# Performance work log

Hardware: AMD Instinct MI355X
Metric: run time of the kernel (lower is better)

Reference implementation:

```python
import jax, jax.numpy as jnp
import numpy as np


def _gat_layer(x, W, att_l, att_r, b, src, dst, num_nodes, heads, out_feat, concat):
    # x: [N, in], W: [in, H*F]
    xl = (x @ W).reshape(num_nodes, heads, out_feat)          # [N, H, F]
    a_l = jnp.sum(xl * att_l, axis=2)                          # [N, H]
    a_r = jnp.sum(xl * att_r, axis=2)                          # [N, H]
    # edge scores: alpha_j (source, att_l) + alpha_i (target, att_r)
    e = a_l[src] + a_r[dst]                                    # [E, H]
    e = jax.nn.leaky_relu(e, 0.2)
    # segment softmax over destination-node neighborhoods
    e_max = jax.ops.segment_max(e, dst, num_segments=num_nodes)
    e_exp = jnp.exp(e - e_max[dst])
    denom = jax.ops.segment_sum(e_exp, dst, num_segments=num_nodes)
    alpha = e_exp / (denom[dst] + 1e-16)                       # [E, H]
    # weighted gather + scatter-add aggregation
    msg = alpha[:, :, None] * xl[src]                          # [E, H, F]
    out = jax.ops.segment_sum(msg, dst, num_segments=num_nodes)  # [N, H, F]
    if concat:
        out = out.reshape(num_nodes, heads * out_feat)
    else:
        out = out.mean(axis=1)                                 # [N, F]
    return out + b


def setup_inputs() -> dict:
    key = jax.random.key(0)
    ks = jax.random.split(key, 8)
    N, E = 50000, 800000
    in_dim, hidden, out_dim, H = 128, 8, 64, 8
    x = jax.random.normal(ks[0], (N, in_dim), dtype=jnp.float32)
    edge_index = jax.random.randint(ks[1], (2, E), 0, N, dtype=jnp.int64)
    s = 0.1
    return {
        "x": x,
        "edge_index": edge_index,
        "W1": jax.random.normal(ks[2], (in_dim, hidden * H), dtype=jnp.float32) * s,
        "att_l1": jax.random.normal(ks[3], (1, H, hidden), dtype=jnp.float32) * s,
        "att_r1": jax.random.normal(ks[4], (1, H, hidden), dtype=jnp.float32) * s,
        "b1": jnp.zeros((hidden * H,), dtype=jnp.float32),
        "W2": jax.random.normal(ks[5], (hidden * H, out_dim * H), dtype=jnp.float32) * s,
        "att_l2": jax.random.normal(ks[6], (1, H, out_dim), dtype=jnp.float32) * s,
        "att_r2": jax.random.normal(ks[7], (1, H, out_dim), dtype=jnp.float32) * s,
        "b2": jnp.zeros((1, out_dim), dtype=jnp.float32),
    }


def reference(x, edge_index, W1, att_l1, att_r1, b1, W2, att_l2, att_r2, b2):
    N = x.shape[0]
    H = att_l1.shape[1]
    src, dst = edge_index[0], edge_index[1]
    h = _gat_layer(x, W1, att_l1, att_r1, b1, src, dst, N, H, att_l1.shape[2], concat=True)
    h = jax.nn.relu(h)
    out = _gat_layer(h, W2, att_l2, att_r2, b2, src, dst, N, H, att_l2.shape[2], concat=False)
    return out
```

## Files before the change

kernel.cpp:

```cpp
#include <hip/hip_runtime.h>
#include <stdint.h>

#define NT 256
#define CHUNK 4096
#define BSHIFT 8

typedef __attribute__((ext_vector_type(8))) short bf16x8;
typedef __attribute__((ext_vector_type(4))) float f32x4;

__device__ __forceinline__ float lrelu(float x) { return x > 0.f ? x : 0.2f * x; }

__device__ __forceinline__ float b2f(unsigned short u) {
  union { unsigned int i; float f; } v; v.i = ((unsigned int)u) << 16; return v.f;
}
__device__ __forceinline__ unsigned short f2b(float f) {
  unsigned int u = __float_as_uint(f);
  return (unsigned short)((u + 0x7fffu + ((u >> 16) & 1u)) >> 16);
}

__global__ void detect_kernel(const int* __restrict__ ei, int* __restrict__ flag, int twoE) {
  __shared__ int any;
  if (threadIdx.x == 0) any = 0;
  __syncthreads();
  int n = twoE < 4096 ? twoE : 4096;
  for (int i = threadIdx.x * 2 + 1; i < n; i += 2 * NT)
    if (ei[i] != 0) any = 1;
  __syncthreads();
  if (threadIdx.x == 0) *flag = any;
}

__global__ void cvt_edges_kernel(const void* __restrict__ ei, int* __restrict__ out,
                                 const int* __restrict__ flag, int twoE) {
  int i = blockIdx.x * NT + threadIdx.x;
  if (i >= twoE) return;
  if (*flag) out[i] = ((const int*)ei)[i];
  else       out[i] = (int)((const long long*)ei)[i];
}

__global__ void zero2_kernel(int* __restrict__ a, int* __restrict__ b, int n) {
  int i = blockIdx.x * NT + threadIdx.x;
  if (i < n) { a[i] = 0; b[i] = 0; }
}

__global__ void scan1_kernel(const int* __restrict__ in, int* __restrict__ bsum, int n) {
  __shared__ int sm[NT];
  int idx = blockIdx.x * NT + threadIdx.x;
  sm[threadIdx.x] = (idx < n) ? in[idx] : 0;
  __syncthreads();
  for (int s = NT / 2; s > 0; s >>= 1) {
    if (threadIdx.x < s) sm[threadIdx.x] += sm[threadIdx.x + s];
    __syncthreads();
  }
  if (threadIdx.x == 0) bsum[blockIdx.x] = sm[0];
}

__global__ void scan2_kernel(const int* __restrict__ bsum, int* __restrict__ boff, int SB) {
  __shared__ int sm[NT];
  int t = threadIdx.x;
  int v = (t < SB) ? bsum[t] : 0;
  sm[t] = v;
  __syncthreads();
  for (int s = 1; s < NT; s <<= 1) {
    int add = (t >= s) ? sm[t - s] : 0;
    __syncthreads();
    sm[t] += add;
    __syncthreads();
  }
  if (t < SB) boff[t] = sm[t] - v;
}

__global__ void scan3_kernel(const int* __restrict__ in, const int* __restrict__ boff,
                             int* __restrict__ out, int n) {
  __shared__ int sm[NT];
  int idx = blockIdx.x * NT + threadIdx.x;
  int v = (idx < n) ? in[idx] : 0;
  sm[threadIdx.x] = v;
  __syncthreads();
  for (int s = 1; s < NT; s <<= 1) {
    int add = (threadIdx.x >= s) ? sm[threadIdx.x - s] : 0;
    __syncthreads();
    sm[threadIdx.x] += add;
    __syncthreads();
  }
  if (idx <= n) out[idx] = boff[blockIdx.x] + sm[threadIdx.x] - v;
}

__global__ void bincount_kernel(const int* __restrict__ dst, int* __restrict__ blkcnt,
                                int E, int nblk, int nbk) {
  __shared__ int cnt[256];
  int b = blockIdx.x;
  for (int i = threadIdx.x; i < nbk; i += NT) cnt[i] = 0;
  __syncthreads();
  int beg = b * CHUNK;
  int end = beg + CHUNK < E ? beg + CHUNK : E;
  for (int i = beg + threadIdx.x; i < end; i += NT)
    atomicAdd(&cnt[dst[i] >> BSHIFT], 1);
  __syncthreads();
  for (int i = threadIdx.x; i < nbk; i += NT) blkcnt[i * nblk + b] = cnt[i];
}

__global__ void binwrite_kernel(const int* __restrict__ src, const int* __restrict__ dst,
                                const int* __restrict__ base, long long* __restrict__ binned,
                                int E, int nblk, int nbk) {
  __shared__ int cnt[256];
  int b = blockIdx.x;
  for (int i = threadIdx.x; i < nbk; i += NT) cnt[i] = base[i * nblk + b];
  __syncthreads();
  int beg = b * CHUNK;
  int end = beg + CHUNK < E ? beg + CHUNK : E;
  for (int i = beg + threadIdx.x; i < end; i += NT) {
    int d = dst[i];
    int pos = atomicAdd(&cnt[d >> BSHIFT], 1);
    binned[pos] = ((long long)d << 32) | (unsigned int)src[i];
  }
}

__global__ void deghist_kernel(const long long* __restrict__ binned, int* __restrict__ deg, int E) {
  int e = blockIdx.x * NT + threadIdx.x;
  if (e < E) atomicAdd(&deg[(int)(binned[e] >> 32)], 1);
}

__global__ void scatter2_kernel(const long long* __restrict__ binned, const int* __restrict__ rowptr,
                                int* __restrict__ cursor, int* __restrict__ csr_src, int E) {
  int e = blockIdx.x * NT + threadIdx.x;
  if (e >= E) return;
  long long v = binned[e];
  int d = (int)(v >> 32);
  int s = (int)(v & 0xffffffffLL);
  int pos = rowptr[d] + atomicAdd(&cursor[d], 1);
  csr_src[pos] = s;
}

__global__ void foldB1_kernel(const float* __restrict__ W1, unsigned short* __restrict__ W1pack) {
  int idx = blockIdx.x * NT + threadIdx.x;
  if (idx >= 128 * 64) return;
  int j = idx & 7;
  int lane = (idx >> 3) & 63;
  int ctchunk = idx >> 9;
  int ct = ctchunk & 3;
  int chunk = ctchunk >> 2;
  int k = chunk * 32 + ((lane >> 4) << 3) + j;
  int col = ct * 16 + (lane & 15);
  W1pack[idx] = f2b(W1[k * 64 + col]);
}

__global__ void __launch_bounds__(NT)
gemm1_mfma_kernel(const float* __restrict__ x, const unsigned short* __restrict__ W1pack,
                  const float* __restrict__ attl, const float* __restrict__ attr,
                  unsigned short* __restrict__ xl1b, float* __restrict__ a1, int N) {
  int w = threadIdx.x >> 6;
  int lane = threadIdx.x & 63;
  int colb = lane & 15;
  int rgrp = lane >> 4;
  int row0w = blockIdx.x * 64 + w * 16;
  int arow = row0w + colb;
  if (arow >= N) arow = N - 1;
  const float* ap = x + (size_t)arow * 128 + (rgrp << 3);

  f32x4 acc[4];
#pragma unroll
  for (int ct = 0; ct < 4; ++ct) { acc[ct][0] = 0.f; acc[ct][1] = 0.f; acc[ct][2] = 0.f; acc[ct][3] = 0.f; }

#pragma unroll
  for (int chunk = 0; chunk < 4; ++chunk) {
    float4 v0 = *(const float4*)(ap + chunk * 32);
    float4 v1 = *(const float4*)(ap + chunk * 32 + 4);
    bf16x8 a;
    a[0] = (short)f2b(v0.x); a[1] = (short)f2b(v0.y);
    a[2] = (short)f2b(v0.z); a[3] = (short)f2b(v0.w);
    a[4] = (short)f2b(v1.x); a[5] = (short)f2b(v1.y);
    a[6] = (short)f2b(v1.z); a[7] = (short)f2b(v1.w);
    const unsigned short* bp = W1pack + ((size_t)chunk * 4 * 64 + lane) * 8;
#pragma unroll
    for (int ct = 0; ct < 4; ++ct) {
      bf16x8 b = *(const bf16x8*)(bp + (size_t)ct * 64 * 8);
      acc[ct] = __builtin_amdgcn_mfma_f32_16x16x32_bf16(a, b, acc[ct], 0, 0, 0);
    }
  }

#pragma unroll
  for (int ct = 0; ct < 4; ++ct) {
    float attlc = attl[ct * 16 + colb];
    float attrc = attr[ct * 16 + colb];
    int h = ct * 2 + (colb >> 3);
#pragma unroll
    for (int r = 0; r < 4; ++r) {
      int n = row0w + rgrp * 4 + r;
      float v = acc[ct][r];
      if (n < N) xl1b[(size_t)n * 64 + ct * 16 + colb] = f2b(v);
      float pl = v * attlc;
      float pr = v * attrc;
      pl += __shfl_xor(pl, 1, 64); pr += __shfl_xor(pr, 1, 64);
      pl += __shfl_xor(pl, 2, 64); pr += __shfl_xor(pr, 2, 64);
      pl += __shfl_xor(pl, 4, 64); pr += __shfl_xor(pr, 4, 64);
      if ((lane & 7) == 0 && n < N) {
        a1[n * 16 + h] = pl;
        a1[n * 16 + 8 + h] = pr;
      }
    }
  }
}

__global__ void foldw_kernel(const float* __restrict__ W2, const float* __restrict__ attl2,
                             const float* __restrict__ attr2, float* __restrict__ wl,
                             float* __restrict__ wr) {
  int t = threadIdx.x;
  int k = t >> 3, h = t & 7;
  float sl = 0.f, sr = 0.f;
  for (int f = 0; f < 64; ++f) {
    float w = W2[k * 512 + h * 64 + f];
    sl += w * attl2[h * 64 + f];
    sr += w * attr2[h * 64 + f];
  }
  wl[k * 8 + h] = sl;
  wr[k * 8 + h] = sr;
}

__global__ void foldB_kernel(const float* __restrict__ W2, unsigned short* __restrict__ Bpack) {
  int idx = blockIdx.x * NT + threadIdx.x;
  if (idx >= 512 * 64) return;
  int j = idx & 7;
  int lane = (idx >> 3) & 63;
  int ctchunk = idx >> 9;
  int ct = ctchunk & 3;
  int chunk = ctchunk >> 2;
  int hk = chunk * 32 + ((lane >> 4) << 3) + j;
  int h = hk >> 6, kk = hk & 63;
  int f = ct * 16 + (lane & 15);
  Bpack[idx] = f2b(W2[kk * 512 + h * 64 + f] * 0.125f);
}

__global__ void __launch_bounds__(NT)
node_aggr1_kernel(const int* __restrict__ rowptr, const int* __restrict__ csr_src,
                  const float* __restrict__ a1, const unsigned short* __restrict__ xl1b,
                  const float* __restrict__ b1, unsigned short* __restrict__ hrb, int N) {
  __shared__ float ps[4][64][8];
  __shared__ int ss[4][64];
  int w = threadIdx.x >> 6;
  int n = blockIdx.x * 4 + w;
  if (n >= N) return;
  int lane = threadIdx.x & 63;
  int hstage = lane & 7;
  int j8 = lane >> 3;
  int hown = lane >> 3;
  int base = rowptr[n];
  int deg = rowptr[n + 1] - base;

  float arh = a1[n * 16 + 8 + hstage];
  const unsigned short* xp = xl1b + lane;
  float acc = 0.f, dn = 0.f;

  for (int j0 = 0; j0 < deg; j0 += 64) {
    int cnt = deg - j0; if (cnt > 64) cnt = 64;
    if (lane < cnt) ss[w][lane] = csr_src[base + j0 + lane];
    asm volatile("s_waitcnt lgkmcnt(0)" ::: "memory");
    for (int jj = 0; jj < cnt; jj += 8) {
      int j = jj + j8;
      if (j < cnt) {
        int s = ss[w][j];
        float p = __expf(lrelu(a1[(unsigned)s * 16 + hstage] + arh));
        ps[w][j][hstage] = p;
      }
    }
    asm volatile("s_waitcnt lgkmcnt(0)" ::: "memory");
    int j = 0;
    for (; j + 4 <= cnt; j += 4) {
      int s0 = ss[w][j+0], s1 = ss[w][j+1], s2 = ss[w][j+2], s3 = ss[w][j+3];
      float p0 = ps[w][j+0][hown], p1 = ps[w][j+1][hown];
      float p2 = ps[w][j+2][hown], p3 = ps[w][j+3][hown];
      float v0 = b2f(xp[(unsigned)s0 * 64]), v1 = b2f(xp[(unsigned)s1 * 64]);
      float v2 = b2f(xp[(unsigned)s2 * 64]), v3 = b2f(xp[(unsigned)s3 * 64]);
      dn += (p0 + p1) + (p2 + p3);
      acc += p0 * v0 + p1 * v1 + p2 * v2 + p3 * v3;
    }
    for (; j < cnt; ++j) {
      int s = ss[w][j];
      float p = ps[w][j][hown];
      dn += p;
      acc += p * b2f(xp[(unsigned)s * 64]);
    }
  }
  acc = acc / (dn + 1e-16f);
  float hv = fmaxf(acc + b1[lane], 0.f);
  hrb[(size_t)n * 64 + lane] = f2b(hv);
}

#define A2N 256
__global__ void __launch_bounds__(NT)
a2dots_kernel(const unsigned short* __restrict__ hrb, const float* __restrict__ wl,
              const float* __restrict__ wr, float* __restrict__ a2, int N) {
  __shared__ unsigned short hs[A2N][65];
  __shared__ float wls[64 * 8], wrs[64 * 8];
  int tid = threadIdx.x;
  int n0 = blockIdx.x * A2N;
  for (int i = tid; i < 512; i += NT) { wls[i] = wl[i]; wrs[i] = wr[i]; }
  for (int i = tid; i < A2N * 8; i += NT) {
    int r = i >> 3, seg = i & 7;
    int n = n0 + r;
    uint4 v = make_uint4(0, 0, 0, 0);
    if (n < N) v = *(const uint4*)&hrb[(size_t)n * 64 + seg * 8];
    int c = seg * 8;
    hs[r][c + 0] = (unsigned short)(v.x);
    hs[r][c + 1] = (unsigned short)(v.x >> 16);
    hs[r][c + 2] = (unsigned short)(v.y);
    hs[r][c + 3] = (unsigned short)(v.y >> 16);
    hs[r][c + 4] = (unsigned short)(v.z);
    hs[r][c + 5] = (unsigned short)(v.z >> 16);
    hs[r][c + 6] = (unsigned short)(v.w);
    hs[r][c + 7] = (unsigned short)(v.w >> 16);
  }
  __syncthreads();
  float tl[8], tr[8];
#pragma unroll
  for (int h = 0; h < 8; ++h) { tl[h] = 0.f; tr[h] = 0.f; }
#pragma unroll 4
  for (int k = 0; k < 64; ++k) {
    float hv = b2f(hs[tid][k]);
    float4 l0 = *(const float4*)&wls[k * 8];
    float4 l1 = *(const float4*)&wls[k * 8 + 4];
    float4 r0 = *(const float4*)&wrs[k * 8];
    float4 r1 = *(const float4*)&wrs[k * 8 + 4];
    tl[0] += hv * l0.x; tl[1] += hv * l0.y; tl[2] += hv * l0.z; tl[3] += hv * l0.w;
    tl[4] += hv * l1.x; tl[5] += hv * l1.y; tl[6] += hv * l1.z; tl[7] += hv * l1.w;
    tr[0] += hv * r0.x; tr[1] += hv * r0.y; tr[2] += hv * r0.z; tr[3] += hv * r0.w;
    tr[4] += hv * r1.x; tr[5] += hv * r1.y; tr[6] += hv * r1.z; tr[7] += hv * r1.w;
  }
  int n = n0 + tid;
  if (n < N) {
    *(float4*)&a2[n * 16 + 0]  = make_float4(tl[0], tl[1], tl[2], tl[3]);
    *(float4*)&a2[n * 16 + 4]  = make_float4(tl[4], tl[5], tl[6], tl[7]);
    *(float4*)&a2[n * 16 + 8]  = make_float4(tr[0], tr[1], tr[2], tr[3]);
    *(float4*)&a2[n * 16 + 12] = make_float4(tr[4], tr[5], tr[6], tr[7]);
  }
}

__global__ void __launch_bounds__(NT)
node_aggr2_kernel(const int* __restrict__ rowptr, const int* __restrict__ csr_src,
                  const float* __restrict__ a2, const unsigned short* __restrict__ hrb,
                  unsigned short* __restrict__ gb, int N) {
  __shared__ float ps[4][64][8];
  __shared__ int ss[4][64];
  int w = threadIdx.x >> 6;
  int n = blockIdx.x * 4 + w;
  if (n >= N) return;
  int lane = threadIdx.x & 63;
  int hstage = lane & 7;
  int j8 = lane >> 3;
  int base = rowptr[n];
  int deg = rowptr[n + 1] - base;

  float arh = a2[n * 16 + 8 + hstage];
  const unsigned short* hp = hrb + lane;
  float acc[8] = {0.f, 0.f, 0.f, 0.f, 0.f, 0.f, 0.f, 0.f};
  float dn_own = 0.f;

  for (int j0 = 0; j0 < deg; j0 += 64) {
    int cnt = deg - j0; if (cnt > 64) cnt = 64;
    if (lane < cnt) ss[w][lane] = csr_src[base + j0 + lane];
    asm volatile("s_waitcnt lgkmcnt(0)" ::: "memory");
    for (int jj = 0; jj < cnt; jj += 8) {
      int j = jj + j8;
      if (j < cnt) {
        int s = ss[w][j];
        float p = __expf(lrelu(a2[(unsigned)s * 16 + hstage] + arh));
        ps[w][j][hstage] = p;
      }
    }
    asm volatile("s_waitcnt lgkmcnt(0)" ::: "memory");
    for (int j = 0; j < cnt; ++j) {
      int s = ss[w][j];
      float hv = b2f(hp[(unsigned)s * 64]);
      float4 pa = *(const float4*)&ps[w][j][0];
      float4 pb = *(const float4*)&ps[w][j][4];
      dn_own += ps[w][j][hstage];
      acc[0] += pa.x * hv; acc[1] += pa.y * hv; acc[2] += pa.z * hv; acc[3] += pa.w * hv;
      acc[4] += pb.x * hv; acc[5] += pb.y * hv; acc[6] += pb.z * hv; acc[7] += pb.w * hv;
    }
  }
#pragma unroll
  for (int h = 0; h < 8; ++h) {
    float dnh = __shfl(dn_own, h, 64);
    float v = acc[h] * (1.f / (dnh + 1e-16f));
    gb[(size_t)n * 512 + h * 64 + lane] = f2b(v);
  }
}

__global__ void __launch_bounds__(NT)
gemm3_mfma_kernel(const unsigned short* __restrict__ gb,
                  const unsigned short* __restrict__ Bpack,
                  const float* __restrict__ b2, float* __restrict__ out, int N) {
  int w = threadIdx.x >> 6;
  int lane = threadIdx.x & 63;
  int row0w = blockIdx.x * 64 + w * 16;
  int arow = row0w + (lane & 15);
  if (arow >= N) arow = N - 1;
  const unsigned short* ap = gb + (size_t)arow * 512 + ((lane >> 4) << 3);

  f32x4 acc[4];
#pragma unroll
  for (int ct = 0; ct < 4; ++ct) {
    float bb = b2[ct * 16 + (lane & 15)];
    acc[ct][0] = bb; acc[ct][1] = bb; acc[ct][2] = bb; acc[ct][3] = bb;
  }

#pragma unroll 4
  for (int chunk = 0; chunk < 16; ++chunk) {
    bf16x8 a = *(const bf16x8*)(ap + chunk * 32);
    const unsigned short* bp = Bpack + ((size_t)chunk * 4 * 64 + lane) * 8;
#pragma unroll
    for (int ct = 0; ct < 4; ++ct) {
      bf16x8 b = *(const bf16x8*)(bp + (size_t)ct * 64 * 8);
      acc[ct] = __builtin_amdgcn_mfma_f32_16x16x32_bf16(a, b, acc[ct], 0, 0, 0);
    }
  }

  int orow0 = row0w + ((lane >> 4) << 2);
#pragma unroll
  for (int ct = 0; ct < 4; ++ct) {
    int col = ct * 16 + (lane & 15);
#pragma unroll
    for (int r = 0; r < 4; ++r) {
      int n = orow0 + r;
      if (n < N) out[(size_t)n * 64 + col] = acc[ct][r];
    }
  }
}

extern "C" void kernel_launch(void* const* d_in, const int* in_sizes, int n_in,
                              void* d_out, int out_size, void* d_ws, size_t ws_size,
                              hipStream_t stream) {
  const float* x     = (const float*)d_in[0];
  const void*  ei    = d_in[1];
  const float* W1    = (const float*)d_in[2];
  const float* attl1 = (const float*)d_in[3];
  const float* attr1 = (const float*)d_in[4];
  const float* b1    = (const float*)d_in[5];
  const float* W2    = (const float*)d_in[6];
  const float* attl2 = (const float*)d_in[7];
  const float* attr2 = (const float*)d_in[8];
  const float* b2    = (const float*)d_in[9];
  float* out = (float*)d_out;

  int N = in_sizes[0] / 128;
  int E = in_sizes[1] / 2;

  int nblk = (E + CHUNK - 1) / CHUNK;
  int nbk  = (N + (1 << BSHIFT) - 1) >> BSHIFT;
  int L    = nbk * nblk;

  char* ws = (char*)d_ws;
  size_t off = 0;
  auto alloc = [&](size_t bytes) {
    char* p = ws + off;
    off += (bytes + 255) & ~size_t(255);
    return p;
  };
  int*            edges   = (int*)alloc((size_t)2 * E * 4);
  int*            flag    = (int*)alloc(256);
  int*            deg     = (int*)alloc((size_t)N * 4);
  int*            cursor  = (int*)alloc((size_t)N * 4);
  int*            rowptr  = (int*)alloc((size_t)(N + 1) * 4);
  int*            bsum    = (int*)alloc(1024);
  int*            boff    = (int*)alloc(1024);
  int*            blkcnt  = (int*)alloc((size_t)L * 4);
  int*            basebuf = (int*)alloc((size_t)(L + 1) * 4);
  int*            bsum2   = (int*)alloc(1024);
  int*            boff2   = (int*)alloc(1024);
  long long*      binned  = (long long*)alloc((size_t)E * 8);
  int*            csr_src = (int*)alloc((size_t)E * 4);
  unsigned short* xl1b    = (unsigned short*)alloc((size_t)N * 64 * 2);
  float*          a1      = (float*)alloc((size_t)N * 16 * 4);
  unsigned short* hrb     = (unsigned short*)alloc((size_t)N * 64 * 2);
  float*          a2      = (float*)alloc((size_t)N * 16 * 4);
  float*          wl      = (float*)alloc(64 * 8 * 4);
  float*          wr      = (float*)alloc(64 * 8 * 4);
  unsigned short* Bpack   = (unsigned short*)alloc(512 * 64 * 2);
  unsigned short* W1pack  = (unsigned short*)alloc(128 * 64 * 2);
  unsigned short* gb      = (unsigned short*)alloc((size_t)N * 512 * 2);
  (void)ws_size;

  const int* srcp = edges;
  const int* dstp = edges + E;
  int SB  = (N + 1 + NT - 1) / NT;
  int SBL = (L + 1 + NT - 1) / NT;

  detect_kernel<<<1, NT, 0, stream>>>((const int*)ei, flag, 2 * E);
  cvt_edges_kernel<<<(2 * E + NT - 1) / NT, NT, 0, stream>>>(ei, edges, flag, 2 * E);
  zero2_kernel<<<(N + NT - 1) / NT, NT, 0, stream>>>(deg, cursor, N);

  bincount_kernel<<<nblk, NT, 0, stream>>>(dstp, blkcnt, E, nblk, nbk);
  scan1_kernel<<<SBL, NT, 0, stream>>>(blkcnt, bsum2, L);
  scan2_kernel<<<1, NT, 0, stream>>>(bsum2, boff2, SBL);
  scan3_kernel<<<SBL, NT, 0, stream>>>(blkcnt, boff2, basebuf, L);
  binwrite_kernel<<<nblk, NT, 0, stream>>>(srcp, dstp, basebuf, binned, E, nblk, nbk);

  deghist_kernel<<<(E + NT - 1) / NT, NT, 0, stream>>>(binned, deg, E);
  scan1_kernel<<<SB, NT, 0, stream>>>(deg, bsum, N);
  scan2_kernel<<<1, NT, 0, stream>>>(bsum, boff, SB);
  scan3_kernel<<<SB, NT, 0, stream>>>(deg, boff, rowptr, N);

  scatter2_kernel<<<(E + NT - 1) / NT, NT, 0, stream>>>(binned, rowptr, cursor, csr_src, E);

  foldB1_kernel<<<(128 * 64 + NT - 1) / NT, NT, 0, stream>>>(W1, W1pack);
  gemm1_mfma_kernel<<<(N + 63) / 64, NT, 0, stream>>>(x, W1pack, attl1, attr1, xl1b, a1, N);
  foldw_kernel<<<1, 512, 0, stream>>>(W2, attl2, attr2, wl, wr);
  foldB_kernel<<<(512 * 64 + NT - 1) / NT, NT, 0, stream>>>(W2, Bpack);

  node_aggr1_kernel<<<(N + 3) / 4, NT, 0, stream>>>(rowptr, csr_src, a1, xl1b, b1, hrb, N);

  a2dots_kernel<<<(N + A2N - 1) / A2N, NT, 0, stream>>>(hrb, wl, wr, a2, N);

  node_aggr2_kernel<<<(N + 3) / 4, NT, 0, stream>>>(rowptr, csr_src, a2, hrb, gb, N);
  gemm3_mfma_kernel<<<(N + 63) / 64, NT, 0, stream>>>(gb, Bpack, b2, out, N);
}
```

Measured before the change: 219.6 us.

## Fuse layer-2 aggregation with output GEMM and merge edge conversion into bincount

The layer-2 neighbor aggregation now writes its bf16 rows into shared memory, one 16-row tile per block. The same block then runs the MFMA projection to 64 outputs, so the N×512 intermediate buffer is never written to or read back from global memory. Separately, edge dtype conversion is folded into the destination-bin counting kernel, which removes one launch and one pass over the edge list. The costs are fewer, larger blocks with more shared memory (lower occupancy), and each wave now processes 4 nodes serially, which can expose latency.

After: 252.6 us. 1.15x slower.

```diff
diff --git a/kernel.cpp b/kernel.cpp
--- a/kernel.cpp
+++ b/kernel.cpp
@@ -29,12 +29,26 @@
   if (threadIdx.x == 0) *flag = any;
 }
 
-__global__ void cvt_edges_kernel(const void* __restrict__ ei, int* __restrict__ out,
-                                 const int* __restrict__ flag, int twoE) {
-  int i = blockIdx.x * NT + threadIdx.x;
-  if (i >= twoE) return;
-  if (*flag) out[i] = ((const int*)ei)[i];
-  else       out[i] = (int)((const long long*)ei)[i];
+__global__ void cvtbin_kernel(const void* __restrict__ ei, const int* __restrict__ flag,
+                              int* __restrict__ edges, int* __restrict__ blkcnt,
+                              int E, int nblk, int nbk) {
+  __shared__ int cnt[256];
+  int b = blockIdx.x;
+  for (int i = threadIdx.x; i < nbk; i += NT) cnt[i] = 0;
+  __syncthreads();
+  int beg = b * CHUNK;
+  int end = beg + CHUNK < E ? beg + CHUNK : E;
+  bool is32 = (*flag != 0);
+  for (int i = beg + threadIdx.x; i < end; i += NT) {
+    int s, d;
+    if (is32) { s = ((const int*)ei)[i]; d = ((const int*)ei)[E + i]; }
+    else      { s = (int)((const long long*)ei)[i]; d = (int)((const long long*)ei)[E + i]; }
+    edges[i] = s;
+    edges[E + i] = d;
+    atomicAdd(&cnt[d >> BSHIFT], 1);
+  }
+  __syncthreads();
+  for (int i = threadIdx.x; i < nbk; i += NT) blkcnt[i * nblk + b] = cnt[i];
 }
 
 __global__ void zero2_kernel(int* __restrict__ a, int* __restrict__ b, int n) {
@@ -83,20 +97,6 @@
     __syncthreads();
   }
   if (idx <= n) out[idx] = boff[blockIdx.x] + sm[threadIdx.x] - v;
-}
-
-__global__ void bincount_kernel(const int* __restrict__ dst, int* __restrict__ blkcnt,
-                                int E, int nblk, int nbk) {
-  __shared__ int cnt[256];
-  int b = blockIdx.x;
-  for (int i = threadIdx.x; i < nbk; i += NT) cnt[i] = 0;
-  __syncthreads();
-  int beg = b * CHUNK;
-  int end = beg + CHUNK < E ? beg + CHUNK : E;
-  for (int i = beg + threadIdx.x; i < end; i += NT)
-    atomicAdd(&cnt[dst[i] >> BSHIFT], 1);
-  __syncthreads();
-  for (int i = threadIdx.x; i < nbk; i += NT) blkcnt[i * nblk + b] = cnt[i];
 }
 
 __global__ void binwrite_kernel(const int* __restrict__ src, const int* __restrict__ dst,
@@ -335,94 +335,83 @@
 }
 
 __global__ void __launch_bounds__(NT)
-node_aggr2_kernel(const int* __restrict__ rowptr, const int* __restrict__ csr_src,
-                  const float* __restrict__ a2, const unsigned short* __restrict__ hrb,
-                  unsigned short* __restrict__ gb, int N) {
+node_aggr2_fused_kernel(const int* __restrict__ rowptr, const int* __restrict__ csr_src,
+                        const float* __restrict__ a2, const unsigned short* __restrict__ hrb,
+                        const unsigned short* __restrict__ Bpack, const float* __restrict__ b2,
+                        float* __restrict__ out, int N) {
   __shared__ float ps[4][64][8];
   __shared__ int ss[4][64];
+  __shared__ unsigned short gs[16][520];
   int w = threadIdx.x >> 6;
-  int n = blockIdx.x * 4 + w;
-  if (n >= N) return;
   int lane = threadIdx.x & 63;
   int hstage = lane & 7;
   int j8 = lane >> 3;
-  int base = rowptr[n];
-  int deg = rowptr[n + 1] - base;
-
-  float arh = a2[n * 16 + 8 + hstage];
-  const unsigned short* hp = hrb + lane;
-  float acc[8] = {0.f, 0.f, 0.f, 0.f, 0.f, 0.f, 0.f, 0.f};
-  float dn_own = 0.f;
-
-  for (int j0 = 0; j0 < deg; j0 += 64) {
-    int cnt = deg - j0; if (cnt > 64) cnt = 64;
-    if (lane < cnt) ss[w][lane] = csr_src[base + j0 + lane];
-    asm volatile("s_waitcnt lgkmcnt(0)" ::: "memory");
-    for (int jj = 0; jj < cnt; jj += 8) {
-      int j = jj + j8;
-      if (j < cnt) {
-        int s = ss[w][j];
-        float p = __expf(lrelu(a2[(unsigned)s * 16 + hstage] + arh));
-        ps[w][j][hstage] = p;
+
+  for (int nr = 0; nr < 4; ++nr) {
+    int row = w * 4 + nr;
+    int n = blockIdx.x * 16 + row;
+    if (n < N) {
+      int base = rowptr[n];
+      int deg = rowptr[n + 1] - base;
+      float arh = a2[n * 16 + 8 + hstage];
+      const unsigned short* hp = hrb + lane;
+      float acc[8] = {0.f, 0.f, 0.f, 0.f, 0.f, 0.f, 0.f, 0.f};
+      float dn_own = 0.f;
+
+      for (int j0 = 0; j0 < deg; j0 += 64) {
+        int cnt = deg - j0; if (cnt > 64) cnt = 64;
+        if (lane < cnt) ss[w][lane] = csr_src[base + j0 + lane];
+        asm volatile("s_waitcnt lgkmcnt(0)" ::: "memory");
+        for (int jj = 0; jj < cnt; jj += 8) {
+          int j = jj + j8;
+          if (j < cnt) {
+            int s = ss[w][j];
+            float p = __expf(lrelu(a2[(unsigned)s * 16 + hstage] + arh));
+            ps[w][j][hstage] = p;
+          }
+        }
+        asm volatile("s_waitcnt lgkmcnt(0)" ::: "memory");
+        for (int j = 0; j < cnt; ++j) {
+          int s = ss[w][j];
+          float hv = b2f(hp[(unsigned)s * 64]);
+          float4 pa = *(const float4*)&ps[w][j][0];
+          float4 pb = *(const float4*)&ps[w][j][4];
+          dn_own += ps[w][j][hstage];
+          acc[0] += pa.x * hv; acc[1] += pa.y * hv; acc[2] += pa.z * hv; acc[3] += pa.w * hv;
+          acc[4] += pb.x * hv; acc[5] += pb.y * hv; acc[6] += pb.z * hv; acc[7] += pb.w * hv;
+        }
       }
+#pragma unroll
+      for (int h = 0; h < 8; ++h) {
+        float dnh = __shfl(dn_own, h, 64);
+        float v = acc[h] * (1.f / (dnh + 1e-16f));
+        gs[row][h * 64 + lane] = f2b(v);
+      }
+    } else {
+#pragma unroll
+      for (int h = 0; h < 8; ++h) gs[row][h * 64 + lane] = 0;
     }
-    asm volatile("s_waitcnt lgkmcnt(0)" ::: "memory");
-    for (int j = 0; j < cnt; ++j) {
-      int s = ss[w][j];
-      float hv = b2f(hp[(unsigned)s * 64]);
-      float4 pa = *(const float4*)&ps[w][j][0];
-      float4 pb = *(const float4*)&ps[w][j][4];
-      dn_own += ps[w][j][hstage];
-      acc[0] += pa.x * hv; acc[1] += pa.y * hv; acc[2] += pa.z * hv; acc[3] += pa.w * hv;
-      acc[4] += pb.x * hv; acc[5] += pb.y * hv; acc[6] += pb.z * hv; acc[7] += pb.w * hv;
-    }
-  }
-#pragma unroll
-  for (int h = 0; h < 8; ++h) {
-    float dnh = __shfl(dn_own, h, 64);
-    float v = acc[h] * (1.f / (dnh + 1e-16f));
-    gb[(size_t)n * 512 + h * 64 + lane] = f2b(v);
-  }
-}
-
-__global__ void __launch_bounds__(NT)
-gemm3_mfma_kernel(const unsigned short* __restrict__ gb,
-                  const unsigned short* __restrict__ Bpack,
-                  const float* __restrict__ b2, float* __restrict__ out, int N) {
-  int w = threadIdx.x >> 6;
-  int lane = threadIdx.x & 63;
-  int row0w = blockIdx.x * 64 + w * 16;
-  int arow = row0w + (lane & 15);
-  if (arow >= N) arow = N - 1;
-  const unsigned short* ap = gb + (size_t)arow * 512 + ((lane >> 4) << 3);
-
-  f32x4 acc[4];
-#pragma unroll
-  for (int ct = 0; ct < 4; ++ct) {
-    float bb = b2[ct * 16 + (lane & 15)];
-    acc[ct][0] = bb; acc[ct][1] = bb; acc[ct][2] = bb; acc[ct][3] = bb;
-  }
-
-#pragma unroll 4
+  }
+  __syncthreads();
+
+  f32x4 acc4;
+  {
+    float bb = b2[w * 16 + (lane & 15)];
+    acc4[0] = bb; acc4[1] = bb; acc4[2] = bb; acc4[3] = bb;
+  }
+  const unsigned short* ap = &gs[lane & 15][(lane >> 4) << 3];
+#pragma unroll
   for (int chunk = 0; chunk < 16; ++chunk) {
     bf16x8 a = *(const bf16x8*)(ap + chunk * 32);
-    const unsigned short* bp = Bpack + ((size_t)chunk * 4 * 64 + lane) * 8;
-#pragma unroll
-    for (int ct = 0; ct < 4; ++ct) {
-      bf16x8 b = *(const bf16x8*)(bp + (size_t)ct * 64 * 8);
-      acc[ct] = __builtin_amdgcn_mfma_f32_16x16x32_bf16(a, b, acc[ct], 0, 0, 0);
-    }
-  }
-
-  int orow0 = row0w + ((lane >> 4) << 2);
-#pragma unroll
-  for (int ct = 0; ct < 4; ++ct) {
-    int col = ct * 16 + (lane & 15);
-#pragma unroll
-    for (int r = 0; r < 4; ++r) {
-      int n = orow0 + r;
-      if (n < N) out[(size_t)n * 64 + col] = acc[ct][r];
-    }
+    bf16x8 b = *(const bf16x8*)(Bpack + ((size_t)(chunk * 4 + w) * 64 + lane) * 8);
+    acc4 = __builtin_amdgcn_mfma_f32_16x16x32_bf16(a, b, acc4, 0, 0, 0);
+  }
+  int col = w * 16 + (lane & 15);
+  int orow0 = (lane >> 4) << 2;
+#pragma unroll
+  for (int r = 0; r < 4; ++r) {
+    int n = blockIdx.x * 16 + orow0 + r;
+    if (n < N) out[(size_t)n * 64 + col] = acc4[r];
   }
 }
 
@@ -476,7 +465,6 @@
   float*          wr      = (float*)alloc(64 * 8 * 4);
   unsigned short* Bpack   = (unsigned short*)alloc(512 * 64 * 2);
   unsigned short* W1pack  = (unsigned short*)alloc(128 * 64 * 2);
-  unsigned short* gb      = (unsigned short*)alloc((size_t)N * 512 * 2);
   (void)ws_size;
 
   const int* srcp = edges;
@@ -485,10 +473,9 @@
   int SBL = (L + 1 + NT - 1) / NT;
 
   detect_kernel<<<1, NT, 0, stream>>>((const int*)ei, flag, 2 * E);
-  cvt_edges_kernel<<<(2 * E + NT - 1) / NT, NT, 0, stream>>>(ei, edges, flag, 2 * E);
   zero2_kernel<<<(N + NT - 1) / NT, NT, 0, stream>>>(deg, cursor, N);
 
-  bincount_kernel<<<nblk, NT, 0, stream>>>(dstp, blkcnt, E, nblk, nbk);
+  cvtbin_kernel<<<nblk, NT, 0, stream>>>(ei, flag, edges, blkcnt, E, nblk, nbk);
   scan1_kernel<<<SBL, NT, 0, stream>>>(blkcnt, bsum2, L);
   scan2_kernel<<<1, NT, 0, stream>>>(bsum2, boff2, SBL);
   scan3_kernel<<<SBL, NT, 0, stream>>>(blkcnt, boff2, basebuf, L);
@@ -510,6 +497,5 @@
 
   a2dots_kernel<<<(N + A2N - 1) / A2N, NT, 0, stream>>>(hrb, wl, wr, a2, N);
 
-  node_aggr2_kernel<<<(N + 3) / 4, NT, 0, stream>>>(rowptr, csr_src, a2, hrb, gb, N);
-  gemm3_mfma_kernel<<<(N + 63) / 64, NT, 0, stream>>>(gb, Bpack, b2, out, N);
-}
+  node_aggr2_fused_kernel<<<(N + 15) / 16, NT, 0, stream>>>(rowptr, csr_src, a2, hrb, Bpack, b2, out, N);
+}
```
